# Kernel tuning notes

Measured on AMD Instinct MI355X. Metric: run time of the kernel, lower is better.

## Reference

```python
import jax, jax.numpy as jnp
import numpy as np

B, S, H = 4, 4096, 1024
E, TOP_K, F = 8, 2, 4 * H  # num_experts, top_k, SwiGLU intermediate dim


def setup_inputs() -> dict:
    key = jax.random.key(0)
    k0, k1, k2, k3, k4 = jax.random.split(key, 5)
    init = 0.02  # typical transformer init scale
    return {
        "X": jax.random.normal(k0, (B, S, H), jnp.float32),
        "Wr": jax.random.normal(k1, (H, E), jnp.float32) * init,
        "W1": jax.random.normal(k2, (E, H, F), jnp.float32) * init,  # gate proj
        "W2": jax.random.normal(k3, (E, F, H), jnp.float32) * init,  # down proj
        "W3": jax.random.normal(k4, (E, H, F), jnp.float32) * init,  # up proj
    }


def reference(X, Wr, W1, W2, W3):
    bsz, seq_len, hidden = X.shape
    x = X.reshape(-1, hidden)  # [N, H]
    # Router: softmax over experts, top-k selection, renormalized weights
    router_logits = x @ Wr  # [N, E]
    probs = jax.nn.softmax(router_logits, axis=-1)
    top_w, top_i = jax.lax.top_k(probs, TOP_K)  # [N, K]
    top_w = top_w / jnp.sum(top_w, axis=-1, keepdims=True)
    # Combine: equivalent to the torch gather/index_add dispatch loop.
    # Per-expert dense SwiGLU weighted by the (possibly zero) routing weight.
    out = jnp.zeros_like(x)
    for e in range(E):
        w_e = jnp.sum(jnp.where(top_i == e, top_w, 0.0), axis=-1)  # [N]
        h = (jax.nn.silu(x @ W1[e]) * (x @ W3[e])) @ W2[e]  # [N, H]
        out = out + h * w_e[:, None]
    return out.reshape(bsz, seq_len, hidden), router_logits
```

## Files before the change

### kernel.cpp

```cpp
#include <hip/hip_runtime.h>
#include <hip/hip_bf16.h>

#define NTOK 16384
#define HD 1024
#define NE 8
#define FD 4096
#define BM 128
#define MAXTILES 264

typedef short short8 __attribute__((ext_vector_type(8)));
typedef unsigned short ushort8 __attribute__((ext_vector_type(8)));
typedef float f32x4 __attribute__((ext_vector_type(4)));

__device__ __forceinline__ unsigned short f2bf(float f) {
    unsigned int u = __builtin_bit_cast(unsigned int, f);
    u += 0x7fffu + ((u >> 16) & 1u);
    return (unsigned short)(u >> 16);
}

__global__ void zero16_kernel(uint4* __restrict__ p, int n16) {
    int t = blockIdx.x * 256 + threadIdx.x;
    if (t < n16) p[t] = make_uint4(0u, 0u, 0u, 0u);
}

__global__ __launch_bounds__(256)
void router_kernel(const float* __restrict__ X, const float* __restrict__ Wr,
                   float* __restrict__ logits_out, int* __restrict__ te,
                   float* __restrict__ tw) {
    int wave = threadIdx.x >> 6, lane = threadIdx.x & 63;
    int token = blockIdx.x * 4 + wave;
    const float* x = X + (size_t)token * HD;
    float acc[NE];
#pragma unroll
    for (int e = 0; e < NE; e++) acc[e] = 0.f;
#pragma unroll 4
    for (int j = 0; j < HD / 64; j++) {
        int i = lane + 64 * j;
        float xv = x[i];
        float4 w0 = *(const float4*)(Wr + (size_t)i * NE);
        float4 w1 = *(const float4*)(Wr + (size_t)i * NE + 4);
        acc[0] += xv * w0.x; acc[1] += xv * w0.y;
        acc[2] += xv * w0.z; acc[3] += xv * w0.w;
        acc[4] += xv * w1.x; acc[5] += xv * w1.y;
        acc[6] += xv * w1.z; acc[7] += xv * w1.w;
    }
#pragma unroll
    for (int off = 32; off >= 1; off >>= 1)
#pragma unroll
        for (int e = 0; e < NE; e++)
            acc[e] += __shfl_xor(acc[e], off, 64);
    if (lane < NE) logits_out[(size_t)token * NE + lane] = acc[lane];
    if (lane == 0) {
        int i1 = 0;
#pragma unroll
        for (int e = 1; e < NE; e++) if (acc[e] > acc[i1]) i1 = e;
        int i2 = (i1 == 0) ? 1 : 0;
#pragma unroll
        for (int e = 0; e < NE; e++) if (e != i1 && acc[e] > acc[i2]) i2 = e;
        float w0 = 1.f / (1.f + __expf(acc[i2] - acc[i1]));
        te[token * 2] = i1; te[token * 2 + 1] = i2;
        tw[token * 2] = w0; tw[token * 2 + 1] = 1.f - w0;
    }
}

__global__ void hist_kernel(const int* __restrict__ te, int* __restrict__ meta) {
    __shared__ int c[NE];
    int t = threadIdx.x;
    if (t < NE) c[t] = 0;
    __syncthreads();
    int tok = blockIdx.x * 256 + t;
    atomicAdd(&c[te[tok * 2]], 1);
    atomicAdd(&c[te[tok * 2 + 1]], 1);
    __syncthreads();
    if (t < NE) atomicAdd(&meta[t], c[t]);
}

__global__ void scan_kernel(int* __restrict__ meta) {
    if (threadIdx.x == 0) {
        int* counts = meta;
        int* offs   = meta + 8;
        int* tb     = meta + 17;
        int* cur    = meta + 26;
        offs[0] = 0; tb[0] = 0;
        for (int e = 0; e < NE; e++) {
            offs[e + 1] = offs[e] + counts[e];
            tb[e + 1] = tb[e] + (counts[e] + BM - 1) / BM;
            cur[e] = offs[e];
        }
    }
}

__global__ void scatter_kernel(const int* __restrict__ te, const float* __restrict__ tw,
                               int* __restrict__ meta, int* __restrict__ tok_ids,
                               float* __restrict__ aw) {
    __shared__ int c[NE];
    __shared__ int base[NE];
    int t = threadIdx.x;
    if (t < NE) c[t] = 0;
    __syncthreads();
    int tok = blockIdx.x * 256 + t;
    int e0 = te[tok * 2], e1 = te[tok * 2 + 1];
    int i0 = atomicAdd(&c[e0], 1);
    int i1 = atomicAdd(&c[e1], 1);
    __syncthreads();
    if (t < NE) base[t] = atomicAdd(&meta[26 + t], c[t]);
    __syncthreads();
    int p0 = base[e0] + i0, p1 = base[e1] + i1;
    tok_ids[p0] = tok; aw[p0] = tw[tok * 2];
    tok_ids[p1] = tok; aw[p1] = tw[tok * 2 + 1];
}

__global__ void convert_x_kernel(const float* __restrict__ in, unsigned short* __restrict__ out) {
    size_t t = (size_t)blockIdx.x * 256 + threadIdx.x;
    float4 a = ((const float4*)in)[t * 2];
    float4 b = ((const float4*)in)[t * 2 + 1];
    ushort8 o;
    o[0] = f2bf(a.x); o[1] = f2bf(a.y); o[2] = f2bf(a.z); o[3] = f2bf(a.w);
    o[4] = f2bf(b.x); o[5] = f2bf(b.y); o[6] = f2bf(b.z); o[7] = f2bf(b.w);
    *(ushort8*)(out + t * 8) = o;
}

__global__ __launch_bounds__(256)
void transpose_convert_kernel(const float* __restrict__ in, unsigned short* __restrict__ out,
                              int R, int C) {
    __shared__ float tile[64][65];
    int e = blockIdx.z;
    int c0 = blockIdx.x * 64, r0 = blockIdx.y * 64;
    const float* src = in + (size_t)e * R * C;
    unsigned short* dst = out + (size_t)e * R * C;
    int t = threadIdx.x;
#pragma unroll
    for (int i = 0; i < 4; i++) {
        int idx = t + i * 256;
        int row = idx >> 4, c4 = (idx & 15) * 4;
        float4 v = *(const float4*)(src + (size_t)(r0 + row) * C + c0 + c4);
        tile[row][c4] = v.x; tile[row][c4 + 1] = v.y;
        tile[row][c4 + 2] = v.z; tile[row][c4 + 3] = v.w;
    }
    __syncthreads();
#pragma unroll
    for (int i = 0; i < 2; i++) {
        int idx = t + i * 256;
        int c = idx >> 3, rc = (idx & 7) * 8;
        ushort8 o;
#pragma unroll
        for (int j = 0; j < 8; j++) o[j] = f2bf(tile[rc + j][c]);
        *(ushort8*)(dst + (size_t)(c0 + c) * R + r0 + rc) = o;
    }
}

__global__ __launch_bounds__(256, 2)
void moe_gemm_a(const unsigned short* __restrict__ Xb,
                const unsigned short* __restrict__ W1t,
                const unsigned short* __restrict__ W3t,
                unsigned short* __restrict__ hbuf,
                const int* __restrict__ meta,
                const int* __restrict__ tok_ids,
                int f0, int FC) {
    const int* counts = meta;
    const int* offs = meta + 8;
    const int* tb = meta + 17;
    int bx = blockIdx.x;
    if (bx >= tb[NE]) return;
    int e = 0;
    while (bx >= tb[e + 1]) e++;
    int tIdx = bx - tb[e];
    int rowsBase = offs[e] + tIdx * BM;
    int rowsInTile = counts[e] - tIdx * BM;
    if (rowsInTile > BM) rowsInTile = BM;
    int n0 = blockIdx.y * 64;

    __shared__ unsigned short As[128 * 40];
    __shared__ unsigned short B1s[64 * 40];
    __shared__ unsigned short B3s[64 * 40];

    int t = threadIdx.x;
    int wave = t >> 6, lane = t & 63, q = lane >> 4, m = lane & 15;
    int pos8 = (t & 3) * 8;
    int r0 = t >> 2;
    int rta = min(r0, rowsInTile - 1);
    int rtb = min(64 + r0, rowsInTile - 1);
    int tok_a = tok_ids[rowsBase + rta];
    int tok_b = tok_ids[rowsBase + rtb];
    const unsigned short* apA = Xb + (size_t)tok_a * HD + pos8;
    const unsigned short* apB = Xb + (size_t)tok_b * HD + pos8;
    const unsigned short* bp1 = W1t + ((size_t)e * FD + f0 + n0 + r0) * HD + pos8;
    const unsigned short* bp3 = W3t + ((size_t)e * FD + f0 + n0 + r0) * HD + pos8;
    unsigned short* lwA = As + r0 * 40 + pos8;
    unsigned short* lwB = As + (64 + r0) * 40 + pos8;
    unsigned short* lw1 = B1s + r0 * 40 + pos8;
    unsigned short* lw3 = B3s + r0 * 40 + pos8;

    f32x4 accg[2][4], accu[2][4];
#pragma unroll
    for (int ri = 0; ri < 2; ri++)
#pragma unroll
        for (int ci = 0; ci < 4; ci++) {
            accg[ri][ci] = (f32x4){0.f, 0.f, 0.f, 0.f};
            accu[ri][ci] = (f32x4){0.f, 0.f, 0.f, 0.f};
        }

    for (int kt = 0; kt < HD; kt += 32) {
        uint4 vA = *(const uint4*)(apA + kt);
        uint4 vB = *(const uint4*)(apB + kt);
        uint4 v1 = *(const uint4*)(bp1 + kt);
        uint4 v3 = *(const uint4*)(bp3 + kt);
        __syncthreads();
        *(uint4*)lwA = vA; *(uint4*)lwB = vB;
        *(uint4*)lw1 = v1; *(uint4*)lw3 = v3;
        __syncthreads();
        short8 af[2], b1f[4], b3f[4];
#pragma unroll
        for (int ri = 0; ri < 2; ri++)
            af[ri] = *(const short8*)(As + (wave * 32 + ri * 16 + m) * 40 + q * 8);
#pragma unroll
        for (int ci = 0; ci < 4; ci++) {
            b1f[ci] = *(const short8*)(B1s + (ci * 16 + m) * 40 + q * 8);
            b3f[ci] = *(const short8*)(B3s + (ci * 16 + m) * 40 + q * 8);
        }
#pragma unroll
        for (int ri = 0; ri < 2; ri++)
#pragma unroll
            for (int ci = 0; ci < 4; ci++) {
                accg[ri][ci] = __builtin_amdgcn_mfma_f32_16x16x32_bf16(af[ri], b1f[ci], accg[ri][ci], 0, 0, 0);
                accu[ri][ci] = __builtin_amdgcn_mfma_f32_16x16x32_bf16(af[ri], b3f[ci], accu[ri][ci], 0, 0, 0);
            }
    }
#pragma unroll
    for (int ri = 0; ri < 2; ri++)
#pragma unroll
        for (int ci = 0; ci < 4; ci++)
#pragma unroll
            for (int r = 0; r < 4; r++) {
                int rl = wave * 32 + ri * 16 + q * 4 + r;
                if (rl < rowsInTile) {
                    float g = accg[ri][ci][r], u = accu[ri][ci][r];
                    float hv = g * u / (1.f + __expf(-g));
                    hbuf[(size_t)(rowsBase + rl) * FC + n0 + ci * 16 + m] = f2bf(hv);
                }
            }
}

__global__ __launch_bounds__(256, 2)
void moe_gemm_b(const unsigned short* __restrict__ hbuf,
                const unsigned short* __restrict__ W2t,
                float* __restrict__ out,
                const int* __restrict__ meta,
                const int* __restrict__ tok_ids,
                const float* __restrict__ aw,
                int f0, int FC) {
    const int* counts = meta;
    const int* offs = meta + 8;
    const int* tb = meta + 17;
    int bx = blockIdx.x;
    if (bx >= tb[NE]) return;
    int e = 0;
    while (bx >= tb[e + 1]) e++;
    int tIdx = bx - tb[e];
    int rowsBase = offs[e] + tIdx * BM;
    int rowsInTile = counts[e] - tIdx * BM;
    if (rowsInTile > BM) rowsInTile = BM;
    int n0 = blockIdx.y * 128;

    __shared__ unsigned short As[128 * 40];
    __shared__ unsigned short Bs[128 * 40];

    int t = threadIdx.x;
    int wave = t >> 6, lane = t & 63, q = lane >> 4, m = lane & 15;
    int wr = (wave >> 1) * 64, wc = (wave & 1) * 64;
    int pos8 = (t & 3) * 8;
    int r0 = t >> 2;
    int rta = min(r0, rowsInTile - 1);
    int rtb = min(64 + r0, rowsInTile - 1);
    const unsigned short* apA = hbuf + (size_t)(rowsBase + rta) * FC + pos8;
    const unsigned short* apB = hbuf + (size_t)(rowsBase + rtb) * FC + pos8;
    const unsigned short* bpA = W2t + ((size_t)e * HD + n0 + r0) * FD + f0 + pos8;
    const unsigned short* bpB = W2t + ((size_t)e * HD + n0 + 64 + r0) * FD + f0 + pos8;
    unsigned short* lwA = As + r0 * 40 + pos8;
    unsigned short* lwB = As + (64 + r0) * 40 + pos8;
    unsigned short* lwC = Bs + r0 * 40 + pos8;
    unsigned short* lwD = Bs + (64 + r0) * 40 + pos8;

    f32x4 acc[4][4];
#pragma unroll
    for (int ri = 0; ri < 4; ri++)
#pragma unroll
        for (int ci = 0; ci < 4; ci++) acc[ri][ci] = (f32x4){0.f, 0.f, 0.f, 0.f};

    for (int kt = 0; kt < FC; kt += 32) {
        uint4 vA = *(const uint4*)(apA + kt);
        uint4 vB = *(const uint4*)(apB + kt);
        uint4 vC = *(const uint4*)(bpA + kt);
        uint4 vD = *(const uint4*)(bpB + kt);
        __syncthreads();
        *(uint4*)lwA = vA; *(uint4*)lwB = vB;
        *(uint4*)lwC = vC; *(uint4*)lwD = vD;
        __syncthreads();
        short8 af[4], bf[4];
#pragma unroll
        for (int ri = 0; ri < 4; ri++)
            af[ri] = *(const short8*)(As + (wr + ri * 16 + m) * 40 + q * 8);
#pragma unroll
        for (int ci = 0; ci < 4; ci++)
            bf[ci] = *(const short8*)(Bs + (wc + ci * 16 + m) * 40 + q * 8);
#pragma unroll
        for (int ri = 0; ri < 4; ri++)
#pragma unroll
            for (int ci = 0; ci < 4; ci++)
                acc[ri][ci] = __builtin_amdgcn_mfma_f32_16x16x32_bf16(af[ri], bf[ci], acc[ri][ci], 0, 0, 0);
    }
#pragma unroll
    for (int ri = 0; ri < 4; ri++)
#pragma unroll
        for (int ci = 0; ci < 4; ci++)
#pragma unroll
            for (int r = 0; r < 4; r++) {
                int rl = wr + ri * 16 + q * 4 + r;
                if (rl < rowsInTile) {
                    int arow = rowsBase + rl;
                    int tok = tok_ids[arow];
                    float w = aw[arow];
                    atomicAdd(out + (size_t)tok * HD + n0 + wc + ci * 16 + m,
                              acc[ri][ci][r] * w);
                }
            }
}

extern "C" void kernel_launch(void* const* d_in, const int* in_sizes, int n_in,
                              void* d_out, int out_size, void* d_ws, size_t ws_size,
                              hipStream_t stream) {
    const float* X  = (const float*)d_in[0];
    const float* Wr = (const float*)d_in[1];
    const float* W1 = (const float*)d_in[2];
    const float* W2 = (const float*)d_in[3];
    const float* W3 = (const float*)d_in[4];
    float* out = (float*)d_out;
    float* logits_out = out + (size_t)NTOK * HD;

    char* ws = (char*)d_ws;
    size_t off = 0;
    auto alloc = [&](size_t bytes) -> void* {
        void* p = ws + off;
        off = (off + bytes + 255) & ~(size_t)255;
        return p;
    };
    unsigned short* Xb  = (unsigned short*)alloc((size_t)NTOK * HD * 2);
    unsigned short* W1t = (unsigned short*)alloc((size_t)NE * HD * FD * 2);
    unsigned short* W3t = (unsigned short*)alloc((size_t)NE * HD * FD * 2);
    unsigned short* W2t = (unsigned short*)alloc((size_t)NE * HD * FD * 2);
    int*   tok_ids = (int*)alloc((size_t)NTOK * 2 * 4);
    float* awf     = (float*)alloc((size_t)NTOK * 2 * 4);
    int*   te      = (int*)alloc((size_t)NTOK * 2 * 4);
    float* twf     = (float*)alloc((size_t)NTOK * 2 * 4);
    int*   meta    = (int*)alloc(64 * 4);
    size_t remain = ws_size > off ? ws_size - off : 0;
    int NC = 1;
    while ((size_t)NTOK * 2 * (size_t)(FD / NC) * 2 > remain && NC < 32) NC *= 2;
    int FC = FD / NC;
    unsigned short* hbuf = (unsigned short*)(ws + off);

    zero16_kernel<<<(NTOK * HD * 4 / 16 + 255) / 256, 256, 0, stream>>>((uint4*)out, NTOK * HD * 4 / 16);
    zero16_kernel<<<1, 256, 0, stream>>>((uint4*)meta, 16);

    router_kernel<<<NTOK / 4, 256, 0, stream>>>(X, Wr, logits_out, te, twf);
    hist_kernel<<<NTOK / 256, 256, 0, stream>>>(te, meta);
    scan_kernel<<<1, 64, 0, stream>>>(meta);
    scatter_kernel<<<NTOK / 256, 256, 0, stream>>>(te, twf, meta, tok_ids, awf);

    convert_x_kernel<<<NTOK * HD / 8 / 256, 256, 0, stream>>>(X, Xb);
    transpose_convert_kernel<<<dim3(FD / 64, HD / 64, NE), 256, 0, stream>>>(W1, W1t, HD, FD);
    transpose_convert_kernel<<<dim3(FD / 64, HD / 64, NE), 256, 0, stream>>>(W3, W3t, HD, FD);
    transpose_convert_kernel<<<dim3(HD / 64, FD / 64, NE), 256, 0, stream>>>(W2, W2t, FD, HD);

    for (int c = 0; c < NC; c++) {
        moe_gemm_a<<<dim3(MAXTILES, FC / 64), 256, 0, stream>>>(Xb, W1t, W3t, hbuf, meta, tok_ids, c * FC, FC);
        moe_gemm_b<<<dim3(MAXTILES, HD / 128), 256, 0, stream>>>(hbuf, W2t, out, meta, tok_ids, awf, c * FC, FC);
    }
}
```

Baseline: 1.999 ms.

## Enlarge gate/up GEMM tile to 128x128 and swap grid axes for weight reuse

The gate/up expert GEMM goes from a 128x64 to a 128x128 output tile with a 2x2 wave layout, so each wave computes a 64x64 block and loads A fragments once for twice as many MFMAs. Both expert GEMMs now put the N-tile index on blockIdx.x and the token tile on blockIdx.y, so blocks sharing a token tile are scheduled next to each other and can reuse its rows in cache. The cost is roughly double the accumulator registers (64 f32x4 per thread), which may cut occupancy below the requested two blocks per CU or cause spills, plus larger shared memory per block.

```diff
diff --git a/kernel.cpp b/kernel.cpp
--- a/kernel.cpp
+++ b/kernel.cpp
@@ -160,40 +160,43 @@
     const int* counts = meta;
     const int* offs = meta + 8;
     const int* tb = meta + 17;
-    int bx = blockIdx.x;
-    if (bx >= tb[NE]) return;
+    int by = blockIdx.y;
+    if (by >= tb[NE]) return;
     int e = 0;
-    while (bx >= tb[e + 1]) e++;
-    int tIdx = bx - tb[e];
+    while (by >= tb[e + 1]) e++;
+    int tIdx = by - tb[e];
     int rowsBase = offs[e] + tIdx * BM;
     int rowsInTile = counts[e] - tIdx * BM;
     if (rowsInTile > BM) rowsInTile = BM;
-    int n0 = blockIdx.y * 64;
+    int n0 = blockIdx.x * 128;
 
     __shared__ unsigned short As[128 * 40];
-    __shared__ unsigned short B1s[64 * 40];
-    __shared__ unsigned short B3s[64 * 40];
+    __shared__ unsigned short B1s[128 * 40];
+    __shared__ unsigned short B3s[128 * 40];
 
     int t = threadIdx.x;
     int wave = t >> 6, lane = t & 63, q = lane >> 4, m = lane & 15;
+    int wr = (wave >> 1) * 64, wc = (wave & 1) * 64;
     int pos8 = (t & 3) * 8;
     int r0 = t >> 2;
     int rta = min(r0, rowsInTile - 1);
     int rtb = min(64 + r0, rowsInTile - 1);
-    int tok_a = tok_ids[rowsBase + rta];
-    int tok_b = tok_ids[rowsBase + rtb];
-    const unsigned short* apA = Xb + (size_t)tok_a * HD + pos8;
-    const unsigned short* apB = Xb + (size_t)tok_b * HD + pos8;
-    const unsigned short* bp1 = W1t + ((size_t)e * FD + f0 + n0 + r0) * HD + pos8;
-    const unsigned short* bp3 = W3t + ((size_t)e * FD + f0 + n0 + r0) * HD + pos8;
-    unsigned short* lwA = As + r0 * 40 + pos8;
-    unsigned short* lwB = As + (64 + r0) * 40 + pos8;
-    unsigned short* lw1 = B1s + r0 * 40 + pos8;
-    unsigned short* lw3 = B3s + r0 * 40 + pos8;
-
-    f32x4 accg[2][4], accu[2][4];
-#pragma unroll
-    for (int ri = 0; ri < 2; ri++)
+    const unsigned short* apA = Xb + (size_t)tok_ids[rowsBase + rta] * HD + pos8;
+    const unsigned short* apB = Xb + (size_t)tok_ids[rowsBase + rtb] * HD + pos8;
+    const unsigned short* bp1a = W1t + ((size_t)e * FD + f0 + n0 + r0) * HD + pos8;
+    const unsigned short* bp1b = W1t + ((size_t)e * FD + f0 + n0 + 64 + r0) * HD + pos8;
+    const unsigned short* bp3a = W3t + ((size_t)e * FD + f0 + n0 + r0) * HD + pos8;
+    const unsigned short* bp3b = W3t + ((size_t)e * FD + f0 + n0 + 64 + r0) * HD + pos8;
+    unsigned short* lwA0 = As + r0 * 40 + pos8;
+    unsigned short* lwA1 = As + (64 + r0) * 40 + pos8;
+    unsigned short* lw10 = B1s + r0 * 40 + pos8;
+    unsigned short* lw11 = B1s + (64 + r0) * 40 + pos8;
+    unsigned short* lw30 = B3s + r0 * 40 + pos8;
+    unsigned short* lw31 = B3s + (64 + r0) * 40 + pos8;
+
+    f32x4 accg[4][4], accu[4][4];
+#pragma unroll
+    for (int ri = 0; ri < 4; ri++)
 #pragma unroll
         for (int ci = 0; ci < 4; ci++) {
             accg[ri][ci] = (f32x4){0.f, 0.f, 0.f, 0.f};
@@ -201,25 +204,28 @@
         }
 
     for (int kt = 0; kt < HD; kt += 32) {
-        uint4 vA = *(const uint4*)(apA + kt);
-        uint4 vB = *(const uint4*)(apB + kt);
-        uint4 v1 = *(const uint4*)(bp1 + kt);
-        uint4 v3 = *(const uint4*)(bp3 + kt);
+        uint4 vA0 = *(const uint4*)(apA + kt);
+        uint4 vA1 = *(const uint4*)(apB + kt);
+        uint4 v10 = *(const uint4*)(bp1a + kt);
+        uint4 v11 = *(const uint4*)(bp1b + kt);
+        uint4 v30 = *(const uint4*)(bp3a + kt);
+        uint4 v31 = *(const uint4*)(bp3b + kt);
         __syncthreads();
-        *(uint4*)lwA = vA; *(uint4*)lwB = vB;
-        *(uint4*)lw1 = v1; *(uint4*)lw3 = v3;
+        *(uint4*)lwA0 = vA0; *(uint4*)lwA1 = vA1;
+        *(uint4*)lw10 = v10; *(uint4*)lw11 = v11;
+        *(uint4*)lw30 = v30; *(uint4*)lw31 = v31;
         __syncthreads();
-        short8 af[2], b1f[4], b3f[4];
-#pragma unroll
-        for (int ri = 0; ri < 2; ri++)
-            af[ri] = *(const short8*)(As + (wave * 32 + ri * 16 + m) * 40 + q * 8);
+        short8 af[4], b1f[4], b3f[4];
+#pragma unroll
+        for (int ri = 0; ri < 4; ri++)
+            af[ri] = *(const short8*)(As + (wr + ri * 16 + m) * 40 + q * 8);
 #pragma unroll
         for (int ci = 0; ci < 4; ci++) {
-            b1f[ci] = *(const short8*)(B1s + (ci * 16 + m) * 40 + q * 8);
-            b3f[ci] = *(const short8*)(B3s + (ci * 16 + m) * 40 + q * 8);
+            b1f[ci] = *(const short8*)(B1s + (wc + ci * 16 + m) * 40 + q * 8);
+            b3f[ci] = *(const short8*)(B3s + (wc + ci * 16 + m) * 40 + q * 8);
         }
 #pragma unroll
-        for (int ri = 0; ri < 2; ri++)
+        for (int ri = 0; ri < 4; ri++)
 #pragma unroll
             for (int ci = 0; ci < 4; ci++) {
                 accg[ri][ci] = __builtin_amdgcn_mfma_f32_16x16x32_bf16(af[ri], b1f[ci], accg[ri][ci], 0, 0, 0);
@@ -227,16 +233,16 @@
             }
     }
 #pragma unroll
-    for (int ri = 0; ri < 2; ri++)
+    for (int ri = 0; ri < 4; ri++)
 #pragma unroll
         for (int ci = 0; ci < 4; ci++)
 #pragma unroll
             for (int r = 0; r < 4; r++) {
-                int rl = wave * 32 + ri * 16 + q * 4 + r;
+                int rl = wr + ri * 16 + q * 4 + r;
                 if (rl < rowsInTile) {
                     float g = accg[ri][ci][r], u = accu[ri][ci][r];
                     float hv = g * u / (1.f + __expf(-g));
-                    hbuf[(size_t)(rowsBase + rl) * FC + n0 + ci * 16 + m] = f2bf(hv);
+                    hbuf[(size_t)(rowsBase + rl) * FC + n0 + wc + ci * 16 + m] = f2bf(hv);
                 }
             }
 }
@@ -252,15 +258,15 @@
     const int* counts = meta;
     const int* offs = meta + 8;
     const int* tb = meta + 17;
-    int bx = blockIdx.x;
-    if (bx >= tb[NE]) return;
+    int by = blockIdx.y;
+    if (by >= tb[NE]) return;
     int e = 0;
-    while (bx >= tb[e + 1]) e++;
-    int tIdx = bx - tb[e];
+    while (by >= tb[e + 1]) e++;
+    int tIdx = by - tb[e];
     int rowsBase = offs[e] + tIdx * BM;
     int rowsInTile = counts[e] - tIdx * BM;
     if (rowsInTile > BM) rowsInTile = BM;
-    int n0 = blockIdx.y * 128;
+    int n0 = blockIdx.x * 128;
 
     __shared__ unsigned short As[128 * 40];
     __shared__ unsigned short Bs[128 * 40];
@@ -373,7 +379,7 @@
     transpose_convert_kernel<<<dim3(HD / 64, FD / 64, NE), 256, 0, stream>>>(W2, W2t, FD, HD);
 
     for (int c = 0; c < NC; c++) {
-        moe_gemm_a<<<dim3(MAXTILES, FC / 64), 256, 0, stream>>>(Xb, W1t, W3t, hbuf, meta, tok_ids, c * FC, FC);
-        moe_gemm_b<<<dim3(MAXTILES, HD / 128), 256, 0, stream>>>(hbuf, W2t, out, meta, tok_ids, awf, c * FC, FC);
-    }
-}
+        moe_gemm_a<<<dim3(FC / 128, MAXTILES), 256, 0, stream>>>(Xb, W1t, W3t, hbuf, meta, tok_ids, c * FC, FC);
+        moe_gemm_b<<<dim3(HD / 128, MAXTILES), 256, 0, stream>>>(hbuf, W2t, out, meta, tok_ids, awf, c * FC, FC);
+    }
+}
```

Result: faster. 1.721 ms (-13.9%).
